# Kernel optimization log

Hardware: AMD Instinct MI355X
Metric: run time of the kernel (lower is better)

The kernel has to match this reference:

```python
import jax, jax.numpy as jnp
import numpy as np

D, H, L, P, DFF = 256, 8, 4, 4, 512
HD = D // H
SHAPES = [(128, 128), (64, 64), (32, 32), (16, 16)]


def setup_inputs() -> dict:
    key = jax.random.key(0)
    ks = jax.random.split(key, 16)
    N, Lq = 8, 1000
    Lin = sum(h * w for h, w in SHAPES)
    f = lambda k, s, sc=1.0: jax.random.normal(k, s, dtype=jnp.float32) * sc
    starts = np.cumsum([0] + [h * w for h, w in SHAPES[:-1]])
    return {
        "pre_tgt": f(ks[0], (N, Lq, D)),
        "pre_query_pos": f(ks[1], (N, Lq, D)),
        "src": f(ks[2], (N, Lin, D)),
        "pre_ref_pts": jax.random.uniform(ks[3], (N, Lq, L, 2), dtype=jnp.float32),
        "src_padding_mask": jnp.zeros((N, Lin), dtype=bool),
        "src_spatial_shapes": jnp.array(SHAPES, dtype=jnp.int32),
        "level_start_index": jnp.array(starts, dtype=jnp.int32),
        "W_value": f(ks[4], (D, D), 0.02), "b_value": jnp.zeros((D,), jnp.float32),
        "W_off": f(ks[5], (D, H * L * P * 2), 0.01), "b_off": f(ks[6], (H * L * P * 2,), 0.1),
        "W_attn": f(ks[7], (D, H * L * P), 0.02), "b_attn": jnp.zeros((H * L * P,), jnp.float32),
        "W_out": f(ks[8], (D, D), 0.02), "b_out": jnp.zeros((D,), jnp.float32),
        "g1": jnp.ones((D,), jnp.float32), "be1": jnp.zeros((D,), jnp.float32),
        "W1": f(ks[9], (D, DFF), 0.02), "b1": jnp.zeros((DFF,), jnp.float32),
        "W2": f(ks[10], (DFF, D), 0.02), "b2": jnp.zeros((D,), jnp.float32),
        "g3": jnp.ones((D,), jnp.float32), "be3": jnp.zeros((D,), jnp.float32),
    }


def layernorm(x, g, b):
    m = x.mean(-1, keepdims=True)
    v = x.var(-1, keepdims=True)
    return (x - m) * jax.lax.rsqrt(v + 1e-5) * g + b


def msdeform_attn(query, ref_pts, src, pad_mask, shapes_np,
                  W_value, b_value, W_off, b_off, W_attn, b_attn, W_out, b_out):
    N, Lq, _ = query.shape
    value = src @ W_value + b_value
    value = jnp.where(pad_mask[..., None], 0.0, value)
    value = value.reshape(N, -1, H, HD)
    off = (query @ W_off + b_off).reshape(N, Lq, H, L, P, 2)
    attn = jax.nn.softmax((query @ W_attn + b_attn).reshape(N, Lq, H, L * P), -1)
    attn = attn.reshape(N, Lq, H, L, P)
    # offset normalizer is (W, H) per level
    norm = jnp.asarray(shapes_np[:, [1, 0]], dtype=query.dtype)  # [L,2]
    loc = ref_pts[:, :, None, :, None, :] + off / norm[None, None, None, :, None, :]
    out = jnp.zeros((N, Lq, H, HD), dtype=query.dtype)
    n_idx = jnp.arange(N)[:, None, None, None]
    h_idx = jnp.arange(H)[None, None, :, None]
    start = 0
    for l in range(L):
        Hl, Wl = int(shapes_np[l, 0]), int(shapes_np[l, 1])
        vl = value[:, start:start + Hl * Wl].reshape(N, Hl, Wl, H, HD)
        start += Hl * Wl
        # grid_sample align_corners=False: pixel = loc*size - 0.5, zero padding
        x = loc[:, :, :, l, :, 0] * Wl - 0.5  # [N,Lq,H,P]
        y = loc[:, :, :, l, :, 1] * Hl - 0.5
        x0 = jnp.floor(x); y0 = jnp.floor(y)
        fx = x - x0; fy = y - y0
        x0i = x0.astype(jnp.int32); y0i = y0.astype(jnp.int32)
        samp = jnp.zeros(x.shape + (HD,), dtype=value.dtype)
        for dx, wx in ((0, 1.0 - fx), (1, fx)):
            for dy, wy in ((0, 1.0 - fy), (1, fy)):
                xi = x0i + dx; yi = y0i + dy
                valid = (xi >= 0) & (xi < Wl) & (yi >= 0) & (yi < Hl)
                v = vl[n_idx, jnp.clip(yi, 0, Hl - 1), jnp.clip(xi, 0, Wl - 1), h_idx]
                samp = samp + jnp.where(valid, wx * wy, 0.0)[..., None] * v
        out = out + jnp.einsum('nqhp,nqhpd->nqhd', attn[:, :, :, l], samp)
    return out.reshape(N, Lq, D) @ W_out + b_out


def reference(pre_tgt, pre_query_pos, src, pre_ref_pts, src_padding_mask,
              src_spatial_shapes, level_start_index,
              W_value, b_value, W_off, b_off, W_attn, b_attn, W_out, b_out,
              g1, be1, W1, b1, W2, b2, g3, be3):
    shapes_np = np.asarray(src_spatial_shapes)
    q = pre_tgt + pre_query_pos
    attn_out = msdeform_attn(q, pre_ref_pts, src, src_padding_mask, shapes_np,
                             W_value, b_value, W_off, b_off, W_attn, b_attn, W_out, b_out)
    tgt = layernorm(pre_tgt + attn_out, g1, be1)  # dropout=identity (eval)
    ff = jax.nn.relu(tgt @ W1 + b1) @ W2 + b2
    return layernorm(tgt + ff, g3, be3)
```

## Files before the change

### kernel.cpp

```cpp
#include <hip/hip_runtime.h>
#include <hip/hip_bf16.h>

#define D_MODEL 256
#define NHEAD   8
#define NLEV    4
#define NPTS    4
#define HDIM    32
#define DFFN    512
#define NBATCH  8
#define LQ      1000
#define LIN     21760
#define M_VAL   (NBATCH * LIN)
#define M_Q     (NBATCH * LQ)

typedef __attribute__((ext_vector_type(8))) short short8;
typedef __attribute__((ext_vector_type(4))) short short4v;
typedef __attribute__((ext_vector_type(4))) float f32x4;

struct alignas(8) bf16x4 { __hip_bfloat16 a, b, c, d; };

__device__ __forceinline__ short f2bf(float f) {
    __hip_bfloat16 h = __float2bfloat16(f);
    return *reinterpret_cast<short*>(&h);
}
__device__ __forceinline__ float bf2f(short s) {
    return __uint_as_float(((unsigned)(unsigned short)s) << 16);
}

__global__ __launch_bounds__(256)
void transpose_weights_kernel(const float* __restrict__ Wv, const float* __restrict__ Wo,
                              const float* __restrict__ W1, const float* __restrict__ W2,
                              short* __restrict__ Wv_t, short* __restrict__ Wo_t,
                              short* __restrict__ W1_t, short* __restrict__ W2_t)
{
    const int b = blockIdx.x;
    const float* src; short* dst; int K, N, tb;
    if (b < 64)       { src = Wv; dst = Wv_t; K = 256; N = 256; tb = b; }
    else if (b < 128) { src = Wo; dst = Wo_t; K = 256; N = 256; tb = b - 64; }
    else if (b < 256) { src = W1; dst = W1_t; K = 256; N = 512; tb = b - 128; }
    else              { src = W2; dst = W2_t; K = 512; N = 256; tb = b - 256; }
    const int ntn = N >> 5;
    const int kt = tb / ntn, nt = tb % ntn;
    __shared__ float t[32][33];
    const int x = threadIdx.x & 31, y = threadIdx.x >> 5;
    #pragma unroll
    for (int j = 0; j < 4; ++j)
        t[y + 8*j][x] = src[(kt*32 + y + 8*j) * N + nt*32 + x];
    __syncthreads();
    #pragma unroll
    for (int j = 0; j < 4; ++j)
        dst[(nt*32 + y + 8*j) * K + kt*32 + x] = f2bf(t[x][y + 8*j]);
}

#define BM 64
#define BN 128
#define BK 64

template<bool A_BF16, bool RELU, bool MASK, int OMODE>
__global__ __launch_bounds__(256)
void mfma_gemm_kernel(const void* __restrict__ Ain,
                      const short* __restrict__ Bt,
                      const float* __restrict__ bias,
                      const unsigned char* __restrict__ mask,
                      float* __restrict__ C, __hip_bfloat16* __restrict__ Cb,
                      int M, int N, int K)
{
    __shared__ short As[BM * BK];
    __shared__ short Bs[BN * BK];
    const int tid  = threadIdx.x;
    const int lane = tid & 63, wid = tid >> 6;
    const int wr = wid >> 1, wc = wid & 1;
    const long bm = (long)blockIdx.y * BM;
    const int  bn = blockIdx.x * BN;

    f32x4 acc[2][4];
    #pragma unroll
    for (int m = 0; m < 2; ++m)
        #pragma unroll
        for (int n = 0; n < 4; ++n)
            acc[m][n] = (f32x4){0.f, 0.f, 0.f, 0.f};

    const int arf = tid >> 4;
    const int akf = (tid & 15) * 4;
    const int arh = tid >> 3;
    const int akh = (tid & 7) * 8;

    float4 a_f[4];
    short8 a_h[2];
    short8 b_r[4];

    auto load_tile = [&](int k0) {
        if (!A_BF16) {
            const float* Ap = (const float*)Ain + (long)(k0 + akf);
            #pragma unroll
            for (int i = 0; i < 4; ++i)
                a_f[i] = *reinterpret_cast<const float4*>(Ap + (bm + arf + 16*i) * (long)K);
        } else {
            const short* Ap = (const short*)Ain + (long)(k0 + akh);
            #pragma unroll
            for (int i = 0; i < 2; ++i)
                a_h[i] = *reinterpret_cast<const short8*>(Ap + (bm + arh + 32*i) * (long)K);
        }
        const short* Bp = Bt + (long)(k0 + akh);
        #pragma unroll
        for (int i = 0; i < 4; ++i)
            b_r[i] = *reinterpret_cast<const short8*>(Bp + (bn + arh + 32*i) * (long)K);
    };
    auto store_tile = [&]() {
        if (!A_BF16) {
            #pragma unroll
            for (int i = 0; i < 4; ++i) {
                const int r = arf + 16*i;
                short4v s;
                s[0] = f2bf(a_f[i].x); s[1] = f2bf(a_f[i].y);
                s[2] = f2bf(a_f[i].z); s[3] = f2bf(a_f[i].w);
                *reinterpret_cast<short4v*>(&As[r * BK + (akf ^ ((r & 7) << 3))]) = s;
            }
        } else {
            #pragma unroll
            for (int i = 0; i < 2; ++i) {
                const int r = arh + 32*i;
                *reinterpret_cast<short8*>(&As[r * BK + (akh ^ ((r & 7) << 3))]) = a_h[i];
            }
        }
        #pragma unroll
        for (int i = 0; i < 4; ++i) {
            const int r = arh + 32*i;
            *reinterpret_cast<short8*>(&Bs[r * BK + (akh ^ ((r & 7) << 3))]) = b_r[i];
        }
    };

    load_tile(0);
    const int nsteps = K / BK;
    for (int s = 0; s < nsteps; ++s) {
        store_tile();
        __syncthreads();
        if (s + 1 < nsteps) load_tile((s + 1) * BK);
        #pragma unroll
        for (int kk = 0; kk < 2; ++kk) {
            const int kb = kk * 32 + (lane >> 4) * 8;
            short8 af[2], bfr[4];
            #pragma unroll
            for (int m = 0; m < 2; ++m) {
                const int row = wr * 32 + m * 16 + (lane & 15);
                af[m] = *reinterpret_cast<const short8*>(&As[row * BK + (kb ^ ((row & 7) << 3))]);
            }
            #pragma unroll
            for (int n = 0; n < 4; ++n) {
                const int row = wc * 64 + n * 16 + (lane & 15);
                bfr[n] = *reinterpret_cast<const short8*>(&Bs[row * BK + (kb ^ ((row & 7) << 3))]);
            }
            #pragma unroll
            for (int m = 0; m < 2; ++m)
                #pragma unroll
                for (int n = 0; n < 4; ++n)
                    acc[m][n] = __builtin_amdgcn_mfma_f32_16x16x32_bf16(af[m], bfr[n], acc[m][n], 0, 0, 0);
        }
        __syncthreads();
    }

    #pragma unroll
    for (int m = 0; m < 2; ++m) {
        #pragma unroll
        for (int n = 0; n < 4; ++n) {
            const int col = bn + wc * 64 + n * 16 + (lane & 15);
            const float bc = bias[col];
            #pragma unroll
            for (int r = 0; r < 4; ++r) {
                const long row = bm + wr * 32 + m * 16 + (lane >> 4) * 4 + r;
                float v = acc[m][n][r] + bc;
                if (RELU) v = fmaxf(v, 0.f);
                if (MASK) { if (mask[row]) v = 0.f; }
                if (OMODE == 0)      C[row * (long)N + col] = v;
                else if (OMODE == 1) Cb[row * (long)N + col] = __float2bfloat16(v);
                else {
                    Cb[(size_t)(col >> 5) * ((size_t)M_VAL * HDIM)
                       + (size_t)row * HDIM + (col & 31)] = __float2bfloat16(v);
                }
            }
        }
    }
}

__global__ __launch_bounds__(256)
void proj_gemm_kernel(const float* __restrict__ A, const float* __restrict__ A2,
                      const float* __restrict__ Wo, const float* __restrict__ bo,
                      const float* __restrict__ Wa, const float* __restrict__ ba,
                      float* __restrict__ Co, float* __restrict__ Ca)
{
    __shared__ float As[16][68];
    __shared__ float Bs[16][64];
    const int tid = threadIdx.x;
    const long bm = (long)blockIdx.y * 64;
    const int  bn = blockIdx.x * 64;
    const float* B; const float* bias; float* C; int Nc, cb;
    if (bn < 256) { B = Wo; bias = bo; C = Co; Nc = 256; cb = bn; }
    else          { B = Wa; bias = ba; C = Ca; Nc = 128; cb = bn - 256; }

    const int tx = tid & 15, ty = tid >> 4;
    const int ar = tid >> 2, ac = (tid & 3) * 4;
    float acc[4][4] = {};
    const float* Aptr = A  + (bm + ar) * 256L + ac;
    const float* A2p  = A2 + (bm + ar) * 256L + ac;
    const float* Bptr = B + (long)ty * Nc + cb + tx * 4;

    float4 av, a2, bv;
    auto load = [&](int k0) {
        av = *reinterpret_cast<const float4*>(Aptr + k0);
        a2 = *reinterpret_cast<const float4*>(A2p + k0);
        bv = *reinterpret_cast<const float4*>(Bptr + (long)k0 * Nc);
    };
    load(0);
    for (int k0 = 0; k0 < 256; k0 += 16) {
        As[ac + 0][ar] = av.x + a2.x;
        As[ac + 1][ar] = av.y + a2.y;
        As[ac + 2][ar] = av.z + a2.z;
        As[ac + 3][ar] = av.w + a2.w;
        *reinterpret_cast<float4*>(&Bs[ty][tx * 4]) = bv;
        __syncthreads();
        if (k0 + 16 < 256) load(k0 + 16);
        #pragma unroll
        for (int kk = 0; kk < 16; ++kk) {
            float4 a4 = *reinterpret_cast<const float4*>(&As[kk][ty * 4]);
            float4 b4 = *reinterpret_cast<const float4*>(&Bs[kk][tx * 4]);
            float a[4] = {a4.x, a4.y, a4.z, a4.w};
            float b[4] = {b4.x, b4.y, b4.z, b4.w};
            #pragma unroll
            for (int i = 0; i < 4; ++i)
                #pragma unroll
                for (int j = 0; j < 4; ++j)
                    acc[i][j] = fmaf(a[i], b[j], acc[i][j]);
        }
        __syncthreads();
    }
    const float4 bias4 = *reinterpret_cast<const float4*>(bias + cb + tx * 4);
    #pragma unroll
    for (int i = 0; i < 4; ++i) {
        const long row = bm + ty * 4 + i;
        *reinterpret_cast<float4*>(C + row * Nc + cb + tx * 4) = make_float4(
            acc[i][0] + bias4.x, acc[i][1] + bias4.y,
            acc[i][2] + bias4.z, acc[i][3] + bias4.w);
    }
}

__global__ __launch_bounds__(128)
void msdeform_sample_kernel(const float* __restrict__ off,
                            const float* __restrict__ logits,
                            const float* __restrict__ ref_pts,
                            const __hip_bfloat16* __restrict__ value,
                            __hip_bfloat16* __restrict__ samp)
{
    const int qi = blockIdx.x;
    const int n  = qi / LQ;
    const int t  = threadIdx.x;

    __shared__ int   s_base[128];
    __shared__ float s_wx[128][2];
    __shared__ float s_wy[128][2];

    {
        const int h = t >> 4, lp = t & 15, l = lp >> 2;
        const float lg = logits[qi * 128 + t];
        float mx = lg;
        #pragma unroll
        for (int m = 1; m < 16; m <<= 1) mx = fmaxf(mx, __shfl_xor(mx, m, 64));
        const float e = __expf(lg - mx);
        float ssum = e;
        #pragma unroll
        for (int m = 1; m < 16; m <<= 1) ssum += __shfl_xor(ssum, m, 64);
        const float w = e / ssum;

        const int Wl = 128 >> l;
        constexpr int Start[4] = {0, 16384, 20480, 21504};
        const float x = ref_pts[qi * 8 + l * 2 + 0] * (float)Wl - 0.5f
                      + off[qi * 256 + h * 32 + lp * 2 + 0];
        const float y = ref_pts[qi * 8 + l * 2 + 1] * (float)Wl - 0.5f
                      + off[qi * 256 + h * 32 + lp * 2 + 1];
        const float xf = floorf(x), yf = floorf(y);
        const float fx = x - xf, fy = y - yf;
        const int x0 = (int)xf, y0 = (int)yf;
        const int xb = min(max(x0, 0), Wl - 2);
        const int yb = min(max(y0, 0), Wl - 2);
        const float wx0 = (xb == x0) ? (1.f - fx) : ((xb == x0 + 1) ? fx : 0.f);
        const float wx1 = (xb + 1 == x0) ? (1.f - fx) : ((xb == x0) ? fx : 0.f);
        const float wy0 = w * ((yb == y0) ? (1.f - fy) : ((yb == y0 + 1) ? fy : 0.f));
        const float wy1 = w * ((yb + 1 == y0) ? (1.f - fy) : ((yb == y0) ? fy : 0.f));

        const int row = n * LIN + Start[l] + yb * Wl + xb;
        s_base[t]  = (h * M_VAL + row) * HDIM;
        s_wx[t][0] = wx0; s_wx[t][1] = wx1;
        s_wy[t][0] = wy0; s_wy[t][1] = wy1;
    }
    __syncthreads();

    {
        const int h = t >> 4, cp = t & 15;
        const int side = cp >> 3, ch4 = (cp & 7) * 4;
        float a0 = 0.f, a1 = 0.f, a2 = 0.f, a3 = 0.f;
        #pragma unroll
        for (int lp = 0; lp < 16; ++lp) {
            const int i  = h * 16 + lp;
            const int rs = (128 >> (lp >> 2)) * HDIM;
            const int b  = s_base[i] + side * HDIM + ch4;
            const float wxs = s_wx[i][side];
            const float w0 = wxs * s_wy[i][0];
            const float w1 = wxs * s_wy[i][1];
            const short4v v0 = *reinterpret_cast<const short4v*>(value + b);
            const short4v v1 = *reinterpret_cast<const short4v*>(value + b + rs);
            a0 += w0 * bf2f(v0[0]) + w1 * bf2f(v1[0]);
            a1 += w0 * bf2f(v0[1]) + w1 * bf2f(v1[1]);
            a2 += w0 * bf2f(v0[2]) + w1 * bf2f(v1[2]);
            a3 += w0 * bf2f(v0[3]) + w1 * bf2f(v1[3]);
        }
        a0 += __shfl_xor(a0, 8, 64);
        a1 += __shfl_xor(a1, 8, 64);
        a2 += __shfl_xor(a2, 8, 64);
        a3 += __shfl_xor(a3, 8, 64);
        if (side == 0) {
            bf16x4 o { __float2bfloat16(a0), __float2bfloat16(a1),
                       __float2bfloat16(a2), __float2bfloat16(a3) };
            *reinterpret_cast<bf16x4*>(samp + (long)qi * D_MODEL + h * HDIM + ch4) = o;
        }
    }
}

__global__ __launch_bounds__(256)
void add_ln_kernel(const float* __restrict__ x, const float* __restrict__ y,
                   const float* __restrict__ g, const float* __restrict__ b,
                   float* __restrict__ out)
{
    const int row  = blockIdx.x * 4 + (threadIdx.x >> 6);
    const int lane = threadIdx.x & 63;
    const long base = (long)row * D_MODEL + lane * 4;

    float4 xv = *reinterpret_cast<const float4*>(x + base);
    float4 yv = *reinterpret_cast<const float4*>(y + base);
    float4 v  = make_float4(xv.x + yv.x, xv.y + yv.y, xv.z + yv.z, xv.w + yv.w);

    float sum = v.x + v.y + v.z + v.w;
    float sq  = v.x * v.x + v.y * v.y + v.z * v.z + v.w * v.w;
    #pragma unroll
    for (int m = 1; m < 64; m <<= 1) {
        sum += __shfl_xor(sum, m, 64);
        sq  += __shfl_xor(sq,  m, 64);
    }
    const float mean = sum * (1.f / D_MODEL);
    const float var  = sq * (1.f / D_MODEL) - mean * mean;
    const float rstd = rsqrtf(var + 1e-5f);

    float4 gv = *reinterpret_cast<const float4*>(g + lane * 4);
    float4 bv = *reinterpret_cast<const float4*>(b + lane * 4);
    float4 o;
    o.x = (v.x - mean) * rstd * gv.x + bv.x;
    o.y = (v.y - mean) * rstd * gv.y + bv.y;
    o.z = (v.z - mean) * rstd * gv.z + bv.z;
    o.w = (v.w - mean) * rstd * gv.w + bv.w;
    *reinterpret_cast<float4*>(out + base) = o;
}

extern "C" void kernel_launch(void* const* d_in, const int* in_sizes, int n_in,
                              void* d_out, int out_size, void* d_ws, size_t ws_size,
                              hipStream_t stream)
{
    const float* pre_tgt  = (const float*)d_in[0];
    const float* pre_qpos = (const float*)d_in[1];
    const float* src      = (const float*)d_in[2];
    const float* ref_pts  = (const float*)d_in[3];
    const unsigned char* pad_mask = (const unsigned char*)d_in[4];
    const float* W_value = (const float*)d_in[7];
    const float* b_value = (const float*)d_in[8];
    const float* W_off   = (const float*)d_in[9];
    const float* b_off   = (const float*)d_in[10];
    const float* W_attn  = (const float*)d_in[11];
    const float* b_attn  = (const float*)d_in[12];
    const float* W_out   = (const float*)d_in[13];
    const float* b_out   = (const float*)d_in[14];
    const float* g1      = (const float*)d_in[15];
    const float* be1     = (const float*)d_in[16];
    const float* W1      = (const float*)d_in[17];
    const float* b1      = (const float*)d_in[18];
    const float* W2      = (const float*)d_in[19];
    const float* b2      = (const float*)d_in[20];
    const float* g3      = (const float*)d_in[21];
    const float* be3     = (const float*)d_in[22];
    float* out = (float*)d_out;

    char* w = (char*)d_ws;
    size_t o = 0;
    __hip_bfloat16* value = (__hip_bfloat16*)(w + o); o += (size_t)M_VAL * D_MODEL * 2;
    float* offb    = (float*)(w + o); o += (size_t)M_Q * 256 * 4;
    float* logits  = (float*)(w + o); o += (size_t)M_Q * 128 * 4;
    __hip_bfloat16* samp = (__hip_bfloat16*)(w + o); o += (size_t)M_Q * 256 * 2;
    float* tgt     = (float*)(w + o); o += (size_t)M_Q * 256 * 4;
    short* Wv_t    = (short*)(w + o); o += 256 * 256 * 2;
    short* Wo_t    = (short*)(w + o); o += 256 * 256 * 2;
    short* W1_t    = (short*)(w + o); o += 512 * 256 * 2;
    short* W2_t    = (short*)(w + o); o += 256 * 512 * 2;
    float* attn_out = (float*)w;
    __hip_bfloat16* hidden = (__hip_bfloat16*)(w + 20000000);
    float* ff = offb;

    const dim3 blk(256);

    transpose_weights_kernel<<<dim3(384), blk, 0, stream>>>(
        W_value, W_out, W1, W2, Wv_t, Wo_t, W1_t, W2_t);

    mfma_gemm_kernel<false, false, true, 2><<<dim3(2, M_VAL / BM), blk, 0, stream>>>(
        src, Wv_t, b_value, pad_mask, nullptr, value, M_VAL, 256, 256);

    proj_gemm_kernel<<<dim3(6, M_Q / 64), blk, 0, stream>>>(
        pre_tgt, pre_qpos, W_off, b_off, W_attn, b_attn, offb, logits);

    msdeform_sample_kernel<<<dim3(M_Q), dim3(128), 0, stream>>>(
        offb, logits, ref_pts, value, samp);

    mfma_gemm_kernel<true, false, false, 0><<<dim3(2, M_Q / BM), blk, 0, stream>>>(
        samp, Wo_t, b_out, nullptr, attn_out, nullptr, M_Q, 256, 256);

    add_ln_kernel<<<dim3(M_Q / 4), blk, 0, stream>>>(pre_tgt, attn_out, g1, be1, tgt);

    mfma_gemm_kernel<false, true, false, 1><<<dim3(4, M_Q / BM), blk, 0, stream>>>(
        tgt, W1_t, b1, nullptr, nullptr, hidden, M_Q, 512, 256);

    mfma_gemm_kernel<true, false, false, 0><<<dim3(2, M_Q / BM), blk, 0, stream>>>(
        hidden, W2_t, b2, nullptr, ff, nullptr, M_Q, 256, 512);

    add_ln_kernel<<<dim3(M_Q / 4), blk, 0, stream>>>(tgt, ff, g3, be3, out);
}
```

Baseline: 413.4 us.

## Add weight-resident value GEMM and fuse output/FFN2 GEMMs with add+LayerNorm

Replaces the generic value-projection GEMM with a dedicated kernel that keeps the whole 256x256 bf16 weight in 128KB of dynamic LDS and streams A rows straight from global into registers, two 128-row panels per block. The out-projection and second FFN GEMMs now cover full 256-column rows per block and do bias, residual add and LayerNorm in the epilogue, which removes two add_ln launches and the fp32 intermediate round trips. The generic templated GEMM becomes an FFN1-only kernel. In exchange, the value kernel runs at low occupancy with a large per-block LDS fill, and the fused kernels launch only M_Q/64 blocks.

```diff
diff --git a/kernel.cpp b/kernel.cpp
--- a/kernel.cpp
+++ b/kernel.cpp
@@ -12,6 +12,7 @@
 #define LIN     21760
 #define M_VAL   (NBATCH * LIN)
 #define M_Q     (NBATCH * LQ)
+#define NPANEL  (M_VAL / 128)
 
 typedef __attribute__((ext_vector_type(8))) short short8;
 typedef __attribute__((ext_vector_type(4))) short short4v;
@@ -52,17 +53,90 @@
         dst[(nt*32 + y + 8*j) * K + kt*32 + x] = f2bf(t[x][y + 8*j]);
 }
 
+__global__ __launch_bounds__(512, 2)
+void value_gemm_kernel(const float* __restrict__ src, const short* __restrict__ Bt,
+                       const float* __restrict__ bias, const unsigned char* __restrict__ mask,
+                       __hip_bfloat16* __restrict__ value)
+{
+    extern __shared__ short Bs[];
+    const int tid  = threadIdx.x;
+    const int lane = tid & 63, wid = tid >> 6;
+    const int l15 = lane & 15, l4 = lane >> 4;
+
+    #pragma unroll
+    for (int i = 0; i < 16; ++i) {
+        const int e  = i * 4096 + tid * 8;
+        const int n  = e >> 8, kp = e & 255;
+        const int k  = kp ^ ((n & 7) << 3);
+        *reinterpret_cast<short8*>(&Bs[e]) =
+            *reinterpret_cast<const short8*>(&Bt[n * 256 + k]);
+    }
+    float biasv[16];
+    #pragma unroll
+    for (int n4 = 0; n4 < 16; ++n4) biasv[n4] = bias[n4 * 16 + l15];
+    __syncthreads();
+
+    const int p0   = blockIdx.x * 2;
+    const int rowA = wid * 16 + l15;
+    const int kb0  = l4 * 8;
+
+    float4 A[16];
+    f32x4 acc[16];
+
+    #pragma unroll 1
+    for (int pan = 0; pan < 2; ++pan) {
+        const int p = p0 + pan;
+        const float* ap = src + ((long)(p * 128) + rowA) * 256 + kb0;
+
+        #pragma unroll
+        for (int kk = 0; kk < 8; ++kk) {
+            A[2*kk]   = *reinterpret_cast<const float4*>(ap + kk * 32);
+            A[2*kk+1] = *reinterpret_cast<const float4*>(ap + kk * 32 + 4);
+        }
+        #pragma unroll
+        for (int n4 = 0; n4 < 16; ++n4) acc[n4] = (f32x4){0.f, 0.f, 0.f, 0.f};
+
+        #pragma unroll
+        for (int kk = 0; kk < 8; ++kk) {
+            const float4 lo = A[2*kk], hi = A[2*kk+1];
+            short8 af;
+            af[0] = f2bf(lo.x); af[1] = f2bf(lo.y); af[2] = f2bf(lo.z); af[3] = f2bf(lo.w);
+            af[4] = f2bf(hi.x); af[5] = f2bf(hi.y); af[6] = f2bf(hi.z); af[7] = f2bf(hi.w);
+            const int kb = kk * 32 + kb0;
+            #pragma unroll
+            for (int n4 = 0; n4 < 16; ++n4) {
+                const int nr = n4 * 16 + l15;
+                const short8 bf = *reinterpret_cast<const short8*>(
+                    &Bs[nr * 256 + (kb ^ ((nr & 7) << 3))]);
+                acc[n4] = __builtin_amdgcn_mfma_f32_16x16x32_bf16(af, bf, acc[n4], 0, 0, 0);
+            }
+        }
+
+        const int rbase = p * 128 + wid * 16 + l4 * 4;
+        bool mk[4];
+        #pragma unroll
+        for (int r = 0; r < 4; ++r) mk[r] = mask[rbase + r] != 0;
+        #pragma unroll
+        for (int n4 = 0; n4 < 16; ++n4) {
+            const int col = n4 * 16 + l15;
+            __hip_bfloat16* vp = value + (size_t)(col >> 5) * ((size_t)M_VAL * HDIM) + (col & 31);
+            #pragma unroll
+            for (int r = 0; r < 4; ++r) {
+                float v = acc[n4][r] + biasv[n4];
+                if (mk[r]) v = 0.f;
+                vp[(size_t)(rbase + r) * HDIM] = __float2bfloat16(v);
+            }
+        }
+    }
+}
+
 #define BM 64
 #define BN 128
 #define BK 64
 
-template<bool A_BF16, bool RELU, bool MASK, int OMODE>
 __global__ __launch_bounds__(256)
-void mfma_gemm_kernel(const void* __restrict__ Ain,
-                      const short* __restrict__ Bt,
-                      const float* __restrict__ bias,
-                      const unsigned char* __restrict__ mask,
-                      float* __restrict__ C, __hip_bfloat16* __restrict__ Cb,
+void ffn1_gemm_kernel(const float* __restrict__ Ain, const short* __restrict__ Bt,
+                      const float* __restrict__ bias, __hip_bfloat16* __restrict__ Cb,
                       int M, int N, int K)
 {
     __shared__ short As[BM * BK];
@@ -86,42 +160,26 @@
     const int akh = (tid & 7) * 8;
 
     float4 a_f[4];
-    short8 a_h[2];
     short8 b_r[4];
 
     auto load_tile = [&](int k0) {
-        if (!A_BF16) {
-            const float* Ap = (const float*)Ain + (long)(k0 + akf);
-            #pragma unroll
-            for (int i = 0; i < 4; ++i)
-                a_f[i] = *reinterpret_cast<const float4*>(Ap + (bm + arf + 16*i) * (long)K);
-        } else {
-            const short* Ap = (const short*)Ain + (long)(k0 + akh);
-            #pragma unroll
-            for (int i = 0; i < 2; ++i)
-                a_h[i] = *reinterpret_cast<const short8*>(Ap + (bm + arh + 32*i) * (long)K);
-        }
+        const float* Ap = Ain + (long)(k0 + akf);
+        #pragma unroll
+        for (int i = 0; i < 4; ++i)
+            a_f[i] = *reinterpret_cast<const float4*>(Ap + (bm + arf + 16*i) * (long)K);
         const short* Bp = Bt + (long)(k0 + akh);
         #pragma unroll
         for (int i = 0; i < 4; ++i)
             b_r[i] = *reinterpret_cast<const short8*>(Bp + (bn + arh + 32*i) * (long)K);
     };
     auto store_tile = [&]() {
-        if (!A_BF16) {
-            #pragma unroll
-            for (int i = 0; i < 4; ++i) {
-                const int r = arf + 16*i;
-                short4v s;
-                s[0] = f2bf(a_f[i].x); s[1] = f2bf(a_f[i].y);
-                s[2] = f2bf(a_f[i].z); s[3] = f2bf(a_f[i].w);
-                *reinterpret_cast<short4v*>(&As[r * BK + (akf ^ ((r & 7) << 3))]) = s;
-            }
-        } else {
-            #pragma unroll
-            for (int i = 0; i < 2; ++i) {
-                const int r = arh + 32*i;
-                *reinterpret_cast<short8*>(&As[r * BK + (akh ^ ((r & 7) << 3))]) = a_h[i];
-            }
+        #pragma unroll
+        for (int i = 0; i < 4; ++i) {
+            const int r = arf + 16*i;
+            short4v s;
+            s[0] = f2bf(a_f[i].x); s[1] = f2bf(a_f[i].y);
+            s[2] = f2bf(a_f[i].z); s[3] = f2bf(a_f[i].w);
+            *reinterpret_cast<short4v*>(&As[r * BK + (akf ^ ((r & 7) << 3))]) = s;
         }
         #pragma unroll
         for (int i = 0; i < 4; ++i) {
@@ -168,15 +226,144 @@
             #pragma unroll
             for (int r = 0; r < 4; ++r) {
                 const long row = bm + wr * 32 + m * 16 + (lane >> 4) * 4 + r;
-                float v = acc[m][n][r] + bc;
-                if (RELU) v = fmaxf(v, 0.f);
-                if (MASK) { if (mask[row]) v = 0.f; }
-                if (OMODE == 0)      C[row * (long)N + col] = v;
-                else if (OMODE == 1) Cb[row * (long)N + col] = __float2bfloat16(v);
-                else {
-                    Cb[(size_t)(col >> 5) * ((size_t)M_VAL * HDIM)
-                       + (size_t)row * HDIM + (col & 31)] = __float2bfloat16(v);
-                }
+                float v = fmaxf(acc[m][n][r] + bc, 0.f);
+                Cb[row * (long)N + col] = __float2bfloat16(v);
+            }
+        }
+    }
+}
+
+template<int KDIM>
+__global__ __launch_bounds__(256)
+void gemm_ln_kernel(const __hip_bfloat16* __restrict__ Abf, const short* __restrict__ Bt,
+                    const float* __restrict__ bias, const float* __restrict__ residual,
+                    const float* __restrict__ g, const float* __restrict__ be,
+                    float* __restrict__ out)
+{
+    __shared__ short As[64 * BK];
+    __shared__ short Bs[256 * BK];
+    __shared__ float red[64][4][2];
+    __shared__ float mrs[64][2];
+
+    const int tid  = threadIdx.x;
+    const int lane = tid & 63, wc = tid >> 6;
+    const int l15 = lane & 15, l4 = lane >> 4;
+    const long bm = (long)blockIdx.x * 64;
+
+    f32x4 acc[4][4];
+    #pragma unroll
+    for (int m = 0; m < 4; ++m)
+        #pragma unroll
+        for (int n = 0; n < 4; ++n)
+            acc[m][n] = (f32x4){0.f, 0.f, 0.f, 0.f};
+
+    const int arh = tid >> 3;
+    const int akh = (tid & 7) * 8;
+    const short* Ain = reinterpret_cast<const short*>(Abf);
+
+    short8 a_r[2], b_r[8];
+    auto load_tile = [&](int k0) {
+        const short* Ap = Ain + (long)(k0 + akh);
+        #pragma unroll
+        for (int i = 0; i < 2; ++i)
+            a_r[i] = *reinterpret_cast<const short8*>(Ap + (bm + arh + 32*i) * (long)KDIM);
+        const short* Bp = Bt + (long)(k0 + akh);
+        #pragma unroll
+        for (int i = 0; i < 8; ++i)
+            b_r[i] = *reinterpret_cast<const short8*>(Bp + (arh + 32*i) * (long)KDIM);
+    };
+    auto store_tile = [&]() {
+        #pragma unroll
+        for (int i = 0; i < 2; ++i) {
+            const int r = arh + 32*i;
+            *reinterpret_cast<short8*>(&As[r * BK + (akh ^ ((r & 7) << 3))]) = a_r[i];
+        }
+        #pragma unroll
+        for (int i = 0; i < 8; ++i) {
+            const int r = arh + 32*i;
+            *reinterpret_cast<short8*>(&Bs[r * BK + (akh ^ ((r & 7) << 3))]) = b_r[i];
+        }
+    };
+
+    load_tile(0);
+    #pragma unroll
+    for (int s = 0; s < KDIM / BK; ++s) {
+        store_tile();
+        __syncthreads();
+        if (s + 1 < KDIM / BK) load_tile((s + 1) * BK);
+        #pragma unroll
+        for (int kk = 0; kk < 2; ++kk) {
+            const int kb = kk * 32 + l4 * 8;
+            short8 af[4], bfr[4];
+            #pragma unroll
+            for (int m = 0; m < 4; ++m) {
+                const int row = m * 16 + l15;
+                af[m] = *reinterpret_cast<const short8*>(&As[row * BK + (kb ^ ((row & 7) << 3))]);
+            }
+            #pragma unroll
+            for (int n = 0; n < 4; ++n) {
+                const int row = wc * 64 + n * 16 + l15;
+                bfr[n] = *reinterpret_cast<const short8*>(&Bs[row * BK + (kb ^ ((row & 7) << 3))]);
+            }
+            #pragma unroll
+            for (int m = 0; m < 4; ++m)
+                #pragma unroll
+                for (int n = 0; n < 4; ++n)
+                    acc[m][n] = __builtin_amdgcn_mfma_f32_16x16x32_bf16(af[m], bfr[n], acc[m][n], 0, 0, 0);
+        }
+        __syncthreads();
+    }
+
+    float gv[4], bev[4], bi[4];
+    #pragma unroll
+    for (int n = 0; n < 4; ++n) {
+        const int c = wc * 64 + n * 16 + l15;
+        gv[n] = g[c]; bev[n] = be[c]; bi[n] = bias[c];
+    }
+    #pragma unroll
+    for (int m = 0; m < 4; ++m) {
+        #pragma unroll
+        for (int r = 0; r < 4; ++r) {
+            const int lrow = m * 16 + l4 * 4 + r;
+            const long grow = bm + lrow;
+            float s = 0.f, q = 0.f;
+            #pragma unroll
+            for (int n = 0; n < 4; ++n) {
+                const int c = wc * 64 + n * 16 + l15;
+                float v = acc[m][n][r] + bi[n] + residual[grow * 256 + c];
+                acc[m][n][r] = v;
+                s += v; q += v * v;
+            }
+            #pragma unroll
+            for (int msk = 1; msk < 16; msk <<= 1) {
+                s += __shfl_xor(s, msk, 64);
+                q += __shfl_xor(q, msk, 64);
+            }
+            if (l15 == 0) { red[lrow][wc][0] = s; red[lrow][wc][1] = q; }
+        }
+    }
+    __syncthreads();
+    if (tid < 64) {
+        float S = 0.f, Q = 0.f;
+        #pragma unroll
+        for (int w = 0; w < 4; ++w) { S += red[tid][w][0]; Q += red[tid][w][1]; }
+        const float mean = S * (1.f / 256.f);
+        const float var  = Q * (1.f / 256.f) - mean * mean;
+        mrs[tid][0] = mean;
+        mrs[tid][1] = rsqrtf(var + 1e-5f);
+    }
+    __syncthreads();
+    #pragma unroll
+    for (int m = 0; m < 4; ++m) {
+        #pragma unroll
+        for (int r = 0; r < 4; ++r) {
+            const int lrow = m * 16 + l4 * 4 + r;
+            const long grow = bm + lrow;
+            const float mean = mrs[lrow][0], rs = mrs[lrow][1];
+            #pragma unroll
+            for (int n = 0; n < 4; ++n) {
+                const int c = wc * 64 + n * 16 + l15;
+                out[grow * 256 + c] = (acc[m][n][r] - mean) * rs * gv[n] + bev[n];
             }
         }
     }
@@ -322,40 +509,6 @@
             *reinterpret_cast<bf16x4*>(samp + (long)qi * D_MODEL + h * HDIM + ch4) = o;
         }
     }
-}
-
-__global__ __launch_bounds__(256)
-void add_ln_kernel(const float* __restrict__ x, const float* __restrict__ y,
-                   const float* __restrict__ g, const float* __restrict__ b,
-                   float* __restrict__ out)
-{
-    const int row  = blockIdx.x * 4 + (threadIdx.x >> 6);
-    const int lane = threadIdx.x & 63;
-    const long base = (long)row * D_MODEL + lane * 4;
-
-    float4 xv = *reinterpret_cast<const float4*>(x + base);
-    float4 yv = *reinterpret_cast<const float4*>(y + base);
-    float4 v  = make_float4(xv.x + yv.x, xv.y + yv.y, xv.z + yv.z, xv.w + yv.w);
-
-    float sum = v.x + v.y + v.z + v.w;
-    float sq  = v.x * v.x + v.y * v.y + v.z * v.z + v.w * v.w;
-    #pragma unroll
-    for (int m = 1; m < 64; m <<= 1) {
-        sum += __shfl_xor(sum, m, 64);
-        sq  += __shfl_xor(sq,  m, 64);
-    }
-    const float mean = sum * (1.f / D_MODEL);
-    const float var  = sq * (1.f / D_MODEL) - mean * mean;
-    const float rstd = rsqrtf(var + 1e-5f);
-
-    float4 gv = *reinterpret_cast<const float4*>(g + lane * 4);
-    float4 bv = *reinterpret_cast<const float4*>(b + lane * 4);
-    float4 o;
-    o.x = (v.x - mean) * rstd * gv.x + bv.x;
-    o.y = (v.y - mean) * rstd * gv.y + bv.y;
-    o.z = (v.z - mean) * rstd * gv.z + bv.z;
-    o.w = (v.w - mean) * rstd * gv.w + bv.w;
-    *reinterpret_cast<float4*>(out + base) = o;
 }
 
 extern "C" void kernel_launch(void* const* d_in, const int* in_sizes, int n_in,
@@ -385,6 +538,13 @@
     const float* be3     = (const float*)d_in[22];
     float* out = (float*)d_out;
 
+    static bool attr_set = false;
+    if (!attr_set) {
+        hipFuncSetAttribute((const void*)value_gemm_kernel,
+                            hipFuncAttributeMaxDynamicSharedMemorySize, 131072);
+        attr_set = true;
+    }
+
     char* w = (char*)d_ws;
     size_t o = 0;
     __hip_bfloat16* value = (__hip_bfloat16*)(w + o); o += (size_t)M_VAL * D_MODEL * 2;
@@ -396,17 +556,15 @@
     short* Wo_t    = (short*)(w + o); o += 256 * 256 * 2;
     short* W1_t    = (short*)(w + o); o += 512 * 256 * 2;
     short* W2_t    = (short*)(w + o); o += 256 * 512 * 2;
-    float* attn_out = (float*)w;
     __hip_bfloat16* hidden = (__hip_bfloat16*)(w + 20000000);
-    float* ff = offb;
 
     const dim3 blk(256);
 
     transpose_weights_kernel<<<dim3(384), blk, 0, stream>>>(
         W_value, W_out, W1, W2, Wv_t, Wo_t, W1_t, W2_t);
 
-    mfma_gemm_kernel<false, false, true, 2><<<dim3(2, M_VAL / BM), blk, 0, stream>>>(
-        src, Wv_t, b_value, pad_mask, nullptr, value, M_VAL, 256, 256);
+    value_gemm_kernel<<<dim3(NPANEL / 2), dim3(512), 131072, stream>>>(
+        src, Wv_t, b_value, pad_mask, value);
 
     proj_gemm_kernel<<<dim3(6, M_Q / 64), blk, 0, stream>>>(
         pre_tgt, pre_qpos, W_off, b_off, W_attn, b_attn, offb, logits);
@@ -414,16 +572,12 @@
     msdeform_sample_kernel<<<dim3(M_Q), dim3(128), 0, stream>>>(
         offb, logits, ref_pts, value, samp);
 
-    mfma_gemm_kernel<true, false, false, 0><<<dim3(2, M_Q / BM), blk, 0, stream>>>(
-        samp, Wo_t, b_out, nullptr, attn_out, nullptr, M_Q, 256, 256);
-
-    add_ln_kernel<<<dim3(M_Q / 4), blk, 0, stream>>>(pre_tgt, attn_out, g1, be1, tgt);
-
-    mfma_gemm_kernel<false, true, false, 1><<<dim3(4, M_Q / BM), blk, 0, stream>>>(
-        tgt, W1_t, b1, nullptr, nullptr, hidden, M_Q, 512, 256);
-
-    mfma_gemm_kernel<true, false, false, 0><<<dim3(2, M_Q / BM), blk, 0, stream>>>(
-        hidden, W2_t, b2, nullptr, ff, nullptr, M_Q, 256, 512);
-
-    add_ln_kernel<<<dim3(M_Q / 4), blk, 0, stream>>>(tgt, ff, g3, be3, out);
-}
+    gemm_ln_kernel<256><<<dim3(M_Q / 64), blk, 0, stream>>>(
+        samp, Wo_t, b_out, pre_tgt, g1, be1, tgt);
+
+    ffn1_gemm_kernel<<<dim3(DFFN / BN, M_Q / BM), blk, 0, stream>>>(
+        tgt, W1_t, b1, hidden, M_Q, DFFN, 256);
+
+    gemm_ln_kernel<512><<<dim3(M_Q / 64), blk, 0, stream>>>(
+        hidden, W2_t, b2, tgt, g3, be3, out);
+}
```

Result: slower. 818.1 us (+97.9%).
